# Performance work log

Measured on AMD Instinct MI355X. Metric: run time of the kernel, lower is better.

Reference implementation:

```python
import jax, jax.numpy as jnp
import numpy as np

ALPHA = 0.1


def path_layer(feats, paths, pw, fcW):
    # feats: (N, D); paths: (P, N, L); pw: (L, D); fcW: (D, D)
    gathered = feats[paths]                      # (P, N, L, D) gather
    r = jnp.einsum('pnld,ld->nd', gathered, pw) / paths.shape[0]
    return jax.nn.relu(r @ fcW)


def setup_inputs() -> dict:
    key = jax.random.key(0)
    ks = jax.random.split(key, 16)
    Nm, Nd, D = 8000, 6000, 128
    P, L1, L2, S = 8, 4, 6, 200000
    inp = {
        'paths_mm': jax.random.randint(ks[0], (P, Nm, L1), 0, Nm),
        'paths_dd': jax.random.randint(ks[1], (P, Nd, L1), 0, Nd),
        'paths_md': jax.random.randint(ks[2], (P, Nm + Nd, L2), 0, Nm + Nd),
        'miRNA': jax.random.normal(ks[3], (Nm, Nm), jnp.float32),
        'disease': jax.random.normal(ks[4], (Nd, Nd), jnp.float32),
        'samples': jax.random.randint(ks[5], (S, 2), 0, Nd),
        'Wm': jax.random.normal(ks[6], (Nm, D), jnp.float32) * 0.02,
        'Wd': jax.random.normal(ks[7], (Nd, D), jnp.float32) * 0.02,
        'pw1': jax.random.normal(ks[8], (2, L1, D), jnp.float32) * 0.5,
        'pw2': jax.random.normal(ks[9], (2, L2, D), jnp.float32) * 0.5,
        'fcW': jax.random.normal(ks[10], (2, D, D), jnp.float32) * 0.1,
        'mlpW0': jax.random.normal(ks[11], (4 * D, 256), jnp.float32) * 0.05,
        'mlpb0': jnp.zeros((256,), jnp.float32),
        'mlpW1': jax.random.normal(ks[12], (256, 64), jnp.float32) * 0.05,
        'mlpb1': jnp.zeros((64,), jnp.float32),
        'mlpW2': jax.random.normal(ks[13], (64, 1), jnp.float32) * 0.05,
        'mlpb2': jnp.zeros((1,), jnp.float32),
    }
    return inp


def reference(paths_mm, paths_dd, paths_md, miRNA, disease, samples,
              Wm, Wd, pw1, pw2, fcW, mlpW0, mlpb0, mlpW1, mlpb1, mlpW2, mlpb2):
    num_layers = fcW.shape[0]
    Nm = Wm.shape[0]

    init_m = miRNA @ Wm            # lin_m(miRNA): (Nm, D)
    init_d = disease @ Wd          # lin_d(disease): (Nd, D)

    feats_mm = init_m
    for l in range(num_layers):
        feats_mm = path_layer(feats_mm, paths_mm, pw1[l], fcW[l])
        feats_mm = ALPHA * init_m + (1.0 - ALPHA) * feats_mm

    feats_dd = init_d
    for l in range(num_layers):
        feats_dd = path_layer(feats_dd, paths_dd, pw1[l], fcW[l])
        feats_dd = ALPHA * init_d + (1.0 - ALPHA) * feats_dd

    init_md = jnp.concatenate([init_m, init_d], axis=0)   # (Nm+Nd, D)
    feats_md = init_md
    for l in range(num_layers):
        feats_md = path_layer(feats_md, paths_md, pw2[l], fcW[l])
        feats_md = ALPHA * init_md + (1.0 - ALPHA) * feats_md

    emb_mm = jnp.concatenate([feats_mm, feats_md[:Nm]], axis=1)   # (Nm, 2D)
    emb_dd = jnp.concatenate([feats_dd, feats_md[Nm:]], axis=1)   # (Nd, 2D)

    emb = jnp.concatenate([emb_mm[samples[:, 0]], emb_dd[samples[:, 1]]], axis=1)  # (S, 4D)

    h = jax.nn.relu if False else None  # torch mlp has no activations between linears
    x = emb @ mlpW0 + mlpb0
    x = x @ mlpW1 + mlpb1
    x = x @ mlpW2 + mlpb2
    return jax.nn.sigmoid(x)
```

## Files before the change

### kernel.cpp

```cpp
#include <hip/hip_runtime.h>
#include <hip/hip_bf16.h>
#include <cstdint>
#include <cstddef>

#define ALPHA_ 0.1f

static inline int cdiv(int a, int b) { return (a + b - 1) / b; }

typedef __attribute__((ext_vector_type(8))) short short8;
typedef __attribute__((ext_vector_type(4))) short short4v;
typedef __attribute__((ext_vector_type(4))) float float4v;

struct P8 { float* p[8]; };

__device__ __forceinline__ void gload_lds16(const void* g, void* l) {
  __builtin_amdgcn_global_load_lds((const __attribute__((address_space(1))) unsigned int*)g,
                                   (__attribute__((address_space(3))) unsigned int*)l,
                                   16, 0, 0);
}

__global__ __launch_bounds__(256) void make_wtT(const float* __restrict__ W,
                                                __hip_bfloat16* __restrict__ WtT,
                                                int K)
{
  __shared__ float tile[32][129];
  const int t  = threadIdx.x;
  const int s  = blockIdx.x;
  const int k0 = s * 32;
#pragma unroll
  for (int pass = 0; pass < 4; ++pass) {
    int idx = pass * 1024 + t * 4;
    int k = idx >> 7, c = idx & 127;
    float4v v;
    const float* src = W + (size_t)(k0 + k) * 128 + c;
    if (k0 + k < K) v = *(const float4v*)src;
    else            v = (float4v){0.f, 0.f, 0.f, 0.f};
    tile[k][c] = v.x; tile[k][c + 1] = v.y; tile[k][c + 2] = v.z; tile[k][c + 3] = v.w;
  }
  __syncthreads();
#pragma unroll
  for (int pass = 0; pass < 16; ++pass) {
    int idx = pass * 256 + t;
    int kg = idx >> 10, rem = idx & 1023;
    int c = rem >> 3, e = rem & 7;
    WtT[(size_t)s * 4096 + idx] = __float2bfloat16(tile[kg * 8 + e][c]);
  }
}

template<int KSPLIT>
__global__ __launch_bounds__(512) void init_mfma5(
    const float* __restrict__ Am, const __hip_bfloat16* __restrict__ Wtm, int Nm_, int nbm,
    const float* __restrict__ Ad, const __hip_bfloat16* __restrict__ Wtd, int Nd_, int Kpd,
    P8 parr)
{
  __shared__ __align__(16) __hip_bfloat16 lds_a[128 * 128];
  __shared__ __align__(16) __hip_bfloat16 lds_w[4 * 4096];

  const int t    = threadIdx.x;
  const int lane = t & 63;
  const int wv   = t >> 6;

  const int chunk = blockIdx.x % KSPLIT;
  int mb          = blockIdx.x / KSPLIT;

  const float* A; const __hip_bfloat16* Wt; int N, K, Kpad, rowoff, rb;
  if (mb < nbm) { A = Am; Wt = Wtm; N = Nm_; K = Nm_; Kpad = nbm * 128; rowoff = 0;   rb = mb; }
  else          { A = Ad; Wt = Wtd; N = Nd_; K = Nd_; Kpad = Kpd;       rowoff = Nm_; rb = mb - nbm; }

  float* Cp = parr.p[chunk];

  const int St = Kpad / 128;
  const int s0 = (int)(((long)St * chunk) / KSPLIT);
  const int s1 = (int)(((long)St * (chunk + 1)) / KSPLIT);

  const int row_g0 = rb * 128;

  const float* apass[8];
  int aw_byte[8];
#pragma unroll
  for (int p = 0; p < 8; ++p) {
    int f   = p * 512 + t;
    int row = f >> 5, kq = f & 31;
    int rg  = row_g0 + row; if (rg > N - 1) rg = N - 1;
    apass[p] = A + (size_t)rg * K + kq * 4;
    int c = kq >> 1, h = kq & 1;
    aw_byte[p] = row * 256 + ((c ^ (row & 15)) << 4) + h * 8;
  }

  const int rloc  = lane & 15;
  const int kg    = lane >> 4;
  const int row_l = wv * 16 + rloc;
  int a_rbyte[4];
#pragma unroll
  for (int sub = 0; sub < 4; ++sub) {
    int c = sub * 4 + kg;
    a_rbyte[sub] = row_l * 256 + ((c ^ (row_l & 15)) << 4);
  }
  int w_roff[8];
#pragma unroll
  for (int mt = 0; mt < 8; ++mt)
    w_roff[mt] = (mt * 16 + rloc) * 8;

  float4v acc[8];
#pragma unroll
  for (int mt = 0; mt < 8; ++mt) acc[mt] = (float4v){0.f, 0.f, 0.f, 0.f};

  const char* wt_bytes = (const char*)Wt;

  for (int s = s0; s < s1; ++s) {
#pragma unroll
    for (int i = 0; i < 4; ++i) {
      gload_lds16(wt_bytes + (size_t)(s * 4) * 8192 + (size_t)(i * 512 + wv * 64 + lane) * 16,
                  (char*)lds_w + (size_t)(i * 512 + wv * 64) * 16);
    }
    float4v av[8];
    const int kb = s * 128;
#pragma unroll
    for (int p = 0; p < 8; ++p) {
      const float* src = apass[p] + kb;
      ptrdiff_t rel = (src - A);
      av[p] = *(const float4v*)(A + ((rel > (ptrdiff_t)((size_t)(N) * K - 4)) ? ((size_t)N * K - 4) : rel));
    }
#pragma unroll
    for (int p = 0; p < 8; ++p) {
      union { short4v v; __hip_bfloat16 h[4]; } pk;
      pk.h[0] = __float2bfloat16(av[p].x); pk.h[1] = __float2bfloat16(av[p].y);
      pk.h[2] = __float2bfloat16(av[p].z); pk.h[3] = __float2bfloat16(av[p].w);
      *(short4v*)((char*)lds_a + aw_byte[p]) = pk.v;
    }
    __syncthreads();

#pragma unroll
    for (int sub = 0; sub < 4; ++sub) {
      short8 afrag = *(const short8*)((const char*)lds_a + a_rbyte[sub]);
      const __hip_bfloat16* lw = lds_w + sub * 4096 + kg * 1024;
#pragma unroll
      for (int mt = 0; mt < 8; ++mt) {
        short8 wfrag = *(const short8*)(lw + w_roff[mt]);
        acc[mt] = __builtin_amdgcn_mfma_f32_16x16x32_bf16(wfrag, afrag, acc[mt], 0, 0, 0);
      }
    }
    __syncthreads();
  }

  int row = row_g0 + row_l;
  if (row < N) {
    float* dst = Cp + (size_t)(rowoff + row) * 128 + kg * 4;
#pragma unroll
    for (int mt = 0; mt < 8; ++mt)
      *(float4v*)(dst + mt * 16) = acc[mt];
  }
}

template<int NP>
__global__ __launch_bounds__(256) void combineN(
    P8 parr, float4v* __restrict__ o_init, __hip_bfloat16* __restrict__ state,
    int n4, int NtD)
{
  int i = blockIdx.x * 256 + threadIdx.x;
  if (i >= n4) return;
  float4v s = ((const float4v*)parr.p[0])[i];
#pragma unroll
  for (int j = 1; j < NP; ++j) {
    float4v x = ((const float4v*)parr.p[j])[i];
    s.x += x.x; s.y += x.y; s.z += x.z; s.w += x.w;
  }
  o_init[i] = s;
  union { short4v v; __hip_bfloat16 h[4]; } b;
  b.h[0] = __float2bfloat16(s.x); b.h[1] = __float2bfloat16(s.y);
  b.h[2] = __float2bfloat16(s.z); b.h[3] = __float2bfloat16(s.w);
  *(short4v*)(state + (size_t)i * 4) = b.v;
  *(short4v*)(state + (size_t)NtD + (size_t)i * 4) = b.v;
}

template<int L, int PP>
__device__ __forceinline__ float gath(const __hip_bfloat16* __restrict__ sect,
                                      const int* __restrict__ paths,
                                      const float* __restrict__ pw, int n, int N, int d)
{
  float pwv[L];
#pragma unroll
  for (int l = 0; l < L; ++l) pwv[l] = pw[l * 128 + d];
  float acc = 0.f;
  const int* ip0 = paths + (size_t)n * L;
#pragma unroll
  for (int p = 0; p < PP; ++p) {
    const int* ip = ip0 + (size_t)p * N * L;
    int idx[L];
#pragma unroll
    for (int l = 0; l < L; ++l) idx[l] = ip[l];
#pragma unroll
    for (int l = 0; l < L; ++l)
      acc = fmaf(pwv[l], __bfloat162float(sect[(size_t)idx[l] * 128 + d]), acc);
  }
  return acc;
}

template<int LMM, int LMD, int PP>
__global__ __launch_bounds__(256) void layer_fused(
    const __hip_bfloat16* __restrict__ stateIn,
    const int* __restrict__ paths_mm, const int* __restrict__ paths_dd, const int* __restrict__ paths_md,
    const float* __restrict__ pw1l, const float* __restrict__ pw2l,
    const float* __restrict__ fcWl, const float* __restrict__ initb,
    __hip_bfloat16* __restrict__ stateOut,
    int Nm, int Nd, int nbm, int nbd)
{
  __shared__ float r_lds[16][128];
  const int t  = threadIdx.x;
  const int Nt = Nm + Nd;
  int b = blockIdx.x;

  const __hip_bfloat16* sect; const int* paths; const float* pw;
  int N, rowbase, nb; bool md;
  if (b < nbm)            { sect = stateIn;                     paths = paths_mm; pw = pw1l; N = Nm; rowbase = 0;  nb = b;             md = false; }
  else if (b < nbm + nbd) { sect = stateIn + (size_t)Nm * 128;  paths = paths_dd; pw = pw1l; N = Nd; rowbase = Nm; nb = b - nbm;       md = false; }
  else                    { sect = stateIn + (size_t)Nt * 128;  paths = paths_md; pw = pw2l; N = Nt; rowbase = Nt; nb = b - nbm - nbd; md = true;  }

  const int d   = t & 127;
  const int sub = t >> 7;
  const int n0  = nb * 16;

#pragma unroll
  for (int i = 0; i < 8; ++i) {
    int slot = sub + 2 * i;
    int n = n0 + slot;
    int ng = (n < N) ? n : (N - 1);
    float acc = md ? gath<LMD, PP>(sect, paths, pw, ng, N, d)
                   : gath<LMM, PP>(sect, paths, pw, ng, N, d);
    r_lds[slot][d] = acc * (1.0f / (float)PP);
  }
  __syncthreads();

  const int col = d;
  const int rh  = sub;
  float acc2[8];
#pragma unroll
  for (int j = 0; j < 8; ++j) acc2[j] = 0.f;
#pragma unroll 4
  for (int k = 0; k < 128; k += 8) {
    float w[8];
#pragma unroll
    for (int kk = 0; kk < 8; ++kk) w[kk] = fcWl[(size_t)(k + kk) * 128 + col];
#pragma unroll
    for (int j = 0; j < 8; ++j) {
      const float* rp = &r_lds[rh * 8 + j][k];
#pragma unroll
      for (int kk = 0; kk < 8; ++kk) acc2[j] = fmaf(rp[kk], w[kk], acc2[j]);
    }
  }
#pragma unroll
  for (int j = 0; j < 8; ++j) {
    int n = n0 + rh * 8 + j;
    if (n < N) {
      int rr = rowbase + n;
      int rbase = (rr < Nt) ? rr : rr - Nt;
      float v = ALPHA_ * initb[(size_t)rbase * 128 + col] + (1.f - ALPHA_) * fmaxf(acc2[j], 0.f);
      stateOut[(size_t)rr * 128 + col] = __float2bfloat16(v);
    }
  }
}

__global__ __launch_bounds__(256) void gather_einsum_rt(
    const __hip_bfloat16* __restrict__ feats, const int* __restrict__ paths,
    const float* __restrict__ pw, float* __restrict__ r, int N, int P, int L)
{
  const int d = threadIdx.x & 127;
  const int n = blockIdx.x * 2 + (threadIdx.x >> 7);
  if (n >= N) return;
  float acc = 0.f;
  for (int p = 0; p < P; ++p) {
    const int* ip = paths + ((size_t)p * N + n) * L;
    for (int l = 0; l < L; ++l)
      acc = fmaf(pw[l * 128 + d], __bfloat162float(feats[(size_t)ip[l] * 128 + d]), acc);
  }
  r[(size_t)n * 128 + d] = acc * (1.0f / (float)P);
}

template<int TR>
__global__ __launch_bounds__(256) void fc_all(
    const float* __restrict__ Rm, const float* __restrict__ W,
    const float* __restrict__ initb, __hip_bfloat16* __restrict__ state, int Ntot, int Nt)
{
  const int col = threadIdx.x & 127;
  const int rh  = __builtin_amdgcn_readfirstlane((int)(threadIdx.x >> 7));
  const int row0 = blockIdx.x * (2 * TR) + rh * TR;
  const float* arow[TR];
#pragma unroll
  for (int r = 0; r < TR; ++r) {
    int rr = row0 + r; if (rr > Ntot - 1) rr = Ntot - 1;
    arow[r] = Rm + (size_t)rr * 128;
  }
  float acc[TR];
#pragma unroll
  for (int r = 0; r < TR; ++r) acc[r] = 0.f;
#pragma unroll 4
  for (int k = 0; k < 128; k += 8) {
    float w[8];
#pragma unroll
    for (int kk = 0; kk < 8; ++kk) w[kk] = W[(size_t)(k + kk) * 128 + col];
#pragma unroll
    for (int r = 0; r < TR; ++r) {
      const float* ap = arow[r] + k;
#pragma unroll
      for (int kk = 0; kk < 8; ++kk) acc[r] = fmaf(ap[kk], w[kk], acc[r]);
    }
  }
#pragma unroll
  for (int r = 0; r < TR; ++r) {
    int rr = row0 + r;
    if (rr < Ntot) {
      int rbase = (rr < Nt) ? rr : rr - Nt;
      float v = ALPHA_ * initb[(size_t)rbase * 128 + col] + (1.f - ALPHA_) * fmaxf(acc[r], 0.f);
      state[(size_t)rr * 128 + col] = __float2bfloat16(v);
    }
  }
}

__global__ void collapse1(const float* __restrict__ W0, const float* __restrict__ b0,
                          const float* __restrict__ W1, const float* __restrict__ b1,
                          float* __restrict__ w01, float* __restrict__ b01,
                          int E, int K0, int H1)
{
  int row = blockIdx.x; int c = threadIdx.x;
  if (c >= H1) return;
  const float* src; float base;
  if (row < E) { src = W0 + (size_t)row * K0; base = 0.f; }
  else         { src = b0; base = b1[c]; }
  float a0 = 0.f, a1 = 0.f, a2 = 0.f, a3 = 0.f;
#pragma unroll 4
  for (int k = 0; k < K0; k += 4) {
    a0 = fmaf(src[k + 0], W1[(size_t)(k + 0) * H1 + c], a0);
    a1 = fmaf(src[k + 1], W1[(size_t)(k + 1) * H1 + c], a1);
    a2 = fmaf(src[k + 2], W1[(size_t)(k + 2) * H1 + c], a2);
    a3 = fmaf(src[k + 3], W1[(size_t)(k + 3) * H1 + c], a3);
  }
  float acc = base + ((a0 + a1) + (a2 + a3));
  if (row < E) w01[(size_t)row * H1 + c] = acc; else b01[c] = acc;
}

__global__ void collapse2(const float* __restrict__ w01, const float* __restrict__ b01,
                          const float* __restrict__ W2, const float* __restrict__ b2,
                          float* __restrict__ w512, float* __restrict__ csc,
                          int E, int H1)
{
  int i = blockIdx.x * blockDim.x + threadIdx.x;
  if (i < E) {
    float a0 = 0.f, a1 = 0.f, a2 = 0.f, a3 = 0.f;
    for (int j = 0; j < H1; j += 4) {
      a0 = fmaf(w01[(size_t)i * H1 + j + 0], W2[j + 0], a0);
      a1 = fmaf(w01[(size_t)i * H1 + j + 1], W2[j + 1], a1);
      a2 = fmaf(w01[(size_t)i * H1 + j + 2], W2[j + 2], a2);
      a3 = fmaf(w01[(size_t)i * H1 + j + 3], W2[j + 3], a3);
    }
    w512[i] = (a0 + a1) + (a2 + a3);
  } else if (i == E) {
    float a = b2[0];
    for (int j = 0; j < H1; ++j) a = fmaf(b01[j], W2[j], a);
    csc[0] = a;
  }
}

__global__ __launch_bounds__(256) void node_partial(
    const __hip_bfloat16* __restrict__ Fmm, const __hip_bfloat16* __restrict__ Fdd,
    const __hip_bfloat16* __restrict__ Fmd,
    const float* __restrict__ w512, float* __restrict__ uv, int Nm, int Nt)
{
  int gid = blockIdx.x * blockDim.x + threadIdx.x;
  int wid = gid >> 6;
  int lane = threadIdx.x & 63;
  if (wid >= Nt) return;
  bool isM = wid < Nm;
  const __hip_bfloat16* X = isM ? (Fmm + (size_t)wid * 128) : (Fdd + (size_t)(wid - Nm) * 128);
  const __hip_bfloat16* Y = Fmd + (size_t)wid * 128;
  const float* w1 = w512 + (isM ? 0 : 256);
  const float* w2 = w1 + 128;
  float s = __bfloat162float(X[lane]) * w1[lane];
  s = fmaf(__bfloat162float(X[lane + 64]), w1[lane + 64], s);
  s = fmaf(__bfloat162float(Y[lane]), w2[lane], s);
  s = fmaf(__bfloat162float(Y[lane + 64]), w2[lane + 64], s);
#pragma unroll
  for (int off = 32; off > 0; off >>= 1) s += __shfl_down(s, off);
  if (lane == 0) uv[wid] = s;
}

__global__ __launch_bounds__(256) void score_kernel(
    const int* __restrict__ samples, const float* __restrict__ u, const float* __restrict__ v,
    const float* __restrict__ csc, float* __restrict__ out, int S)
{
  int s = blockIdx.x * blockDim.x + threadIdx.x;
  if (s >= S) return;
  const int2 ij = ((const int2*)samples)[s];
  float x = u[ij.x] + v[ij.y] + csc[0];
  out[s] = 1.0f / (1.0f + expf(-x));
}

extern "C" void kernel_launch(void* const* d_in, const int* in_sizes, int n_in,
                              void* d_out, int out_size, void* d_ws, size_t ws_size,
                              hipStream_t stream)
{
  const int*   paths_mm = (const int*)d_in[0];
  const int*   paths_dd = (const int*)d_in[1];
  const int*   paths_md = (const int*)d_in[2];
  const float* miRNA    = (const float*)d_in[3];
  const float* disease  = (const float*)d_in[4];
  const int*   samples  = (const int*)d_in[5];
  const float* Wm  = (const float*)d_in[6];
  const float* Wd  = (const float*)d_in[7];
  const float* pw1 = (const float*)d_in[8];
  const float* pw2 = (const float*)d_in[9];
  const float* fcW = (const float*)d_in[10];
  const float* W0  = (const float*)d_in[11];
  const float* b0  = (const float*)d_in[12];
  const float* W1  = (const float*)d_in[13];
  const float* b1  = (const float*)d_in[14];
  const float* W2  = (const float*)d_in[15];
  const float* b2  = (const float*)d_in[16];

  const int D  = 128;
  const int Nm = in_sizes[6] / D;
  const int Nd = in_sizes[7] / D;
  const int Nt = Nm + Nd;
  const int S  = in_sizes[5] / 2;
  const int layers = in_sizes[10] / (D * D);
  const int L1 = in_sizes[8] / (layers * D);
  const int L2 = in_sizes[9] / (layers * D);
  const int P  = in_sizes[0] / (Nm * L1);
  const int E  = 4 * D;
  const int K0 = in_sizes[12];
  const int H1 = in_sizes[14];
  const int Kpm = cdiv(Nm, 128) * 128;
  const int Kpd = cdiv(Nd, 128) * 128;
  const size_t NtD = (size_t)Nt * D;

  float* out = (float*)d_out;
  float* ws  = (float*)d_ws;
  size_t off = 0;
  float* init   = ws + off; off += NtD;
  __hip_bfloat16* stateA = (__hip_bfloat16*)(ws + off); off += NtD;
  __hip_bfloat16* stateB = (__hip_bfloat16*)(ws + off); off += NtD;
  float* w01    = ws + off; off += (size_t)E * H1;
  float* b01    = ws + off; off += H1;
  float* w512   = ws + off; off += E;
  float* csc    = ws + off; off += 1;
  float* uv     = ws + off; off += Nt;
  __hip_bfloat16* WtTm = (__hip_bfloat16*)(ws + off); off += (size_t)D * Kpm / 2;
  __hip_bfloat16* WtTd = (__hip_bfloat16*)(ws + off); off += (size_t)D * Kpd / 2;
  float* pextra = ws + off;
  const bool big_ws = (off + 3 * NtD) * 4 <= ws_size;
  (void)n_in; (void)out_size;

  make_wtT<<<Kpm / 32, 256, 0, stream>>>(Wm, WtTm, Nm);
  make_wtT<<<Kpd / 32, 256, 0, stream>>>(Wd, WtTd, Nd);

  collapse1<<<E + 1, 64, 0, stream>>>(W0, b0, W1, b1, w01, b01, E, K0, H1);
  collapse2<<<cdiv(E + 1, 256), 256, 0, stream>>>(w01, b01, W2, b2, w512, csc, E, H1);

  {
    int nbm = Kpm / 128, nbd = cdiv(Nd, 128);
    int n4 = (int)(NtD / 4);
    P8 parr;
    parr.p[0] = init;
    parr.p[1] = (float*)stateB;
    if (big_ws) {
      parr.p[2] = pextra;
      parr.p[3] = pextra + NtD;
      parr.p[4] = pextra + 2 * NtD;
      init_mfma5<5><<<(nbm + nbd) * 5, 512, 0, stream>>>(
          miRNA, WtTm, Nm, nbm, disease, WtTd, Nd, Kpd, parr);
      combineN<5><<<cdiv(n4, 256), 256, 0, stream>>>(parr, (float4v*)init, stateA, n4, (int)NtD);
    } else {
      parr.p[2] = pextra;
      init_mfma5<3><<<(nbm + nbd) * 3, 512, 0, stream>>>(
          miRNA, WtTm, Nm, nbm, disease, WtTd, Nd, Kpd, parr);
      combineN<3><<<cdiv(n4, 256), 256, 0, stream>>>(parr, (float4v*)init, stateA, n4, (int)NtD);
    }
  }

  const bool fuse_ok = (L1 == 4 && L2 == 6 && P == 8 &&
                        Nm % 16 == 0 && Nd % 16 == 0 && Nt % 16 == 0);
  __hip_bfloat16* cur = stateA;
  __hip_bfloat16* nxt = stateB;
  for (int l = 0; l < layers; ++l) {
    const float* pw1l = pw1 + (size_t)l * L1 * D;
    const float* pw2l = pw2 + (size_t)l * L2 * D;
    const float* fcWl = fcW + (size_t)l * D * D;
    if (fuse_ok) {
      int nbm16 = Nm / 16, nbd16 = Nd / 16, nbt16 = Nt / 16;
      layer_fused<4, 6, 8><<<nbm16 + nbd16 + nbt16, 256, 0, stream>>>(
          cur, paths_mm, paths_dd, paths_md, pw1l, pw2l, fcWl, init, nxt,
          Nm, Nd, nbm16, nbd16);
    } else {
      float* bufR = pextra;
      gather_einsum_rt<<<cdiv(Nm, 2), 256, 0, stream>>>(cur, paths_mm, pw1l, bufR, Nm, P, L1);
      gather_einsum_rt<<<cdiv(Nd, 2), 256, 0, stream>>>(cur + (size_t)Nm * D, paths_dd, pw1l,
                                                        bufR + (size_t)Nm * D, Nd, P, L1);
      gather_einsum_rt<<<cdiv(Nt, 2), 256, 0, stream>>>(cur + NtD, paths_md, pw2l,
                                                        bufR + NtD, Nt, P, L2);
      fc_all<8><<<cdiv(2 * Nt, 16), 256, 0, stream>>>(
          bufR, fcWl, init, nxt, 2 * Nt, Nt);
    }
    __hip_bfloat16* tmp = cur; cur = nxt; nxt = tmp;
  }

  node_partial<<<cdiv(Nt * 64, 256), 256, 0, stream>>>(
      cur, cur + (size_t)Nm * D, cur + NtD, w512, uv, Nm, Nt);
  score_kernel<<<cdiv(S, 256), 256, 0, stream>>>(samples, uv, uv + Nm, csc, out, S);
}
```

Measured before the change: 278.3 us.

## Retile init GEMM to 256-row blocks with 64-wide K steps and deeper split-K

```diff
diff --git a/kernel.cpp b/kernel.cpp
--- a/kernel.cpp
+++ b/kernel.cpp
@@ -11,7 +11,7 @@
 typedef __attribute__((ext_vector_type(4))) short short4v;
 typedef __attribute__((ext_vector_type(4))) float float4v;
 
-struct P8 { float* p[8]; };
+struct P12 { float* p[12]; };
 
 __device__ __forceinline__ void gload_lds16(const void* g, void* l) {
   __builtin_amdgcn_global_load_lds((const __attribute__((address_space(1))) unsigned int*)g,
@@ -48,13 +48,13 @@
 }
 
 template<int KSPLIT>
-__global__ __launch_bounds__(512) void init_mfma5(
-    const float* __restrict__ Am, const __hip_bfloat16* __restrict__ Wtm, int Nm_, int nbm,
+__global__ __launch_bounds__(512, 4) void init_mfma6(
+    const float* __restrict__ Am, const __hip_bfloat16* __restrict__ Wtm, int Nm_, int nbm, int Kpm,
     const float* __restrict__ Ad, const __hip_bfloat16* __restrict__ Wtd, int Nd_, int Kpd,
-    P8 parr)
-{
-  __shared__ __align__(16) __hip_bfloat16 lds_a[128 * 128];
-  __shared__ __align__(16) __hip_bfloat16 lds_w[4 * 4096];
+    P12 parr)
+{
+  __shared__ __align__(16) __hip_bfloat16 lds_a[256 * 64];
+  __shared__ __align__(16) __hip_bfloat16 lds_w[2 * 4096];
 
   const int t    = threadIdx.x;
   const int lane = t & 63;
@@ -64,62 +64,66 @@
   int mb          = blockIdx.x / KSPLIT;
 
   const float* A; const __hip_bfloat16* Wt; int N, K, Kpad, rowoff, rb;
-  if (mb < nbm) { A = Am; Wt = Wtm; N = Nm_; K = Nm_; Kpad = nbm * 128; rowoff = 0;   rb = mb; }
-  else          { A = Ad; Wt = Wtd; N = Nd_; K = Nd_; Kpad = Kpd;       rowoff = Nm_; rb = mb - nbm; }
+  if (mb < nbm) { A = Am; Wt = Wtm; N = Nm_; K = Nm_; Kpad = Kpm; rowoff = 0;   rb = mb; }
+  else          { A = Ad; Wt = Wtd; N = Nd_; K = Nd_; Kpad = Kpd; rowoff = Nm_; rb = mb - nbm; }
 
   float* Cp = parr.p[chunk];
 
-  const int St = Kpad / 128;
+  const int St = Kpad / 64;
   const int s0 = (int)(((long)St * chunk) / KSPLIT);
   const int s1 = (int)(((long)St * (chunk + 1)) / KSPLIT);
 
-  const int row_g0 = rb * 128;
+  const int row_g0 = rb * 256;
 
   const float* apass[8];
   int aw_byte[8];
 #pragma unroll
   for (int p = 0; p < 8; ++p) {
     int f   = p * 512 + t;
-    int row = f >> 5, kq = f & 31;
+    int row = f >> 4, kq = f & 15;
     int rg  = row_g0 + row; if (rg > N - 1) rg = N - 1;
     apass[p] = A + (size_t)rg * K + kq * 4;
     int c = kq >> 1, h = kq & 1;
-    aw_byte[p] = row * 256 + ((c ^ (row & 15)) << 4) + h * 8;
-  }
-
-  const int rloc  = lane & 15;
-  const int kg    = lane >> 4;
-  const int row_l = wv * 16 + rloc;
-  int a_rbyte[4];
-#pragma unroll
-  for (int sub = 0; sub < 4; ++sub) {
-    int c = sub * 4 + kg;
-    a_rbyte[sub] = row_l * 256 + ((c ^ (row_l & 15)) << 4);
+    aw_byte[p] = row * 128 + ((c ^ (row & 7)) << 4) + h * 8;
+  }
+
+  const int rloc = lane & 15;
+  const int kg   = lane >> 4;
+  int a_rbyte[2][2];
+#pragma unroll
+  for (int g = 0; g < 2; ++g) {
+    int row_l = wv * 32 + g * 16 + rloc;
+#pragma unroll
+    for (int sub = 0; sub < 2; ++sub) {
+      int c = sub * 4 + kg;
+      a_rbyte[g][sub] = row_l * 128 + ((c ^ (row_l & 7)) << 4);
+    }
   }
   int w_roff[8];
 #pragma unroll
   for (int mt = 0; mt < 8; ++mt)
     w_roff[mt] = (mt * 16 + rloc) * 8;
 
-  float4v acc[8];
-#pragma unroll
-  for (int mt = 0; mt < 8; ++mt) acc[mt] = (float4v){0.f, 0.f, 0.f, 0.f};
+  float4v accA[8], accB[8];
+#pragma unroll
+  for (int mt = 0; mt < 8; ++mt) { accA[mt] = (float4v){0,0,0,0}; accB[mt] = (float4v){0,0,0,0}; }
 
   const char* wt_bytes = (const char*)Wt;
+  const size_t amax = (size_t)N * K - 4;
 
   for (int s = s0; s < s1; ++s) {
 #pragma unroll
-    for (int i = 0; i < 4; ++i) {
-      gload_lds16(wt_bytes + (size_t)(s * 4) * 8192 + (size_t)(i * 512 + wv * 64 + lane) * 16,
-                  (char*)lds_w + (size_t)(i * 512 + wv * 64) * 16);
+    for (int i = 0; i < 2; ++i) {
+      gload_lds16(wt_bytes + (size_t)(s * 2 + i) * 8192 + (size_t)t * 16,
+                  (char*)lds_w + (size_t)i * 8192 + (size_t)(wv * 64) * 16);
     }
     float4v av[8];
-    const int kb = s * 128;
+    const int kb = s * 64;
 #pragma unroll
     for (int p = 0; p < 8; ++p) {
       const float* src = apass[p] + kb;
-      ptrdiff_t rel = (src - A);
-      av[p] = *(const float4v*)(A + ((rel > (ptrdiff_t)((size_t)(N) * K - 4)) ? ((size_t)N * K - 4) : rel));
+      ptrdiff_t rel = src - A;
+      av[p] = *(const float4v*)(A + (((size_t)rel > amax) ? amax : (size_t)rel));
     }
 #pragma unroll
     for (int p = 0; p < 8; ++p) {
@@ -131,30 +135,35 @@
     __syncthreads();
 
 #pragma unroll
-    for (int sub = 0; sub < 4; ++sub) {
-      short8 afrag = *(const short8*)((const char*)lds_a + a_rbyte[sub]);
+    for (int sub = 0; sub < 2; ++sub) {
+      short8 afA = *(const short8*)((const char*)lds_a + a_rbyte[0][sub]);
+      short8 afB = *(const short8*)((const char*)lds_a + a_rbyte[1][sub]);
       const __hip_bfloat16* lw = lds_w + sub * 4096 + kg * 1024;
 #pragma unroll
       for (int mt = 0; mt < 8; ++mt) {
         short8 wfrag = *(const short8*)(lw + w_roff[mt]);
-        acc[mt] = __builtin_amdgcn_mfma_f32_16x16x32_bf16(wfrag, afrag, acc[mt], 0, 0, 0);
+        accA[mt] = __builtin_amdgcn_mfma_f32_16x16x32_bf16(wfrag, afA, accA[mt], 0, 0, 0);
+        accB[mt] = __builtin_amdgcn_mfma_f32_16x16x32_bf16(wfrag, afB, accB[mt], 0, 0, 0);
       }
     }
     __syncthreads();
   }
 
-  int row = row_g0 + row_l;
-  if (row < N) {
-    float* dst = Cp + (size_t)(rowoff + row) * 128 + kg * 4;
-#pragma unroll
-    for (int mt = 0; mt < 8; ++mt)
-      *(float4v*)(dst + mt * 16) = acc[mt];
+#pragma unroll
+  for (int g = 0; g < 2; ++g) {
+    int row = row_g0 + wv * 32 + g * 16 + rloc;
+    if (row < N) {
+      float* dst = Cp + (size_t)(rowoff + row) * 128 + kg * 4;
+#pragma unroll
+      for (int mt = 0; mt < 8; ++mt)
+        *(float4v*)(dst + mt * 16) = (g == 0) ? accA[mt] : accB[mt];
+    }
   }
 }
 
 template<int NP>
 __global__ __launch_bounds__(256) void combineN(
-    P8 parr, float4v* __restrict__ o_init, __hip_bfloat16* __restrict__ state,
+    P12 parr, float4v* __restrict__ o_init, __hip_bfloat16* __restrict__ state,
     int n4, int NtD)
 {
   int i = blockIdx.x * 256 + threadIdx.x;
@@ -428,8 +437,8 @@
   const int E  = 4 * D;
   const int K0 = in_sizes[12];
   const int H1 = in_sizes[14];
-  const int Kpm = cdiv(Nm, 128) * 128;
-  const int Kpd = cdiv(Nd, 128) * 128;
+  const int Kpm = cdiv(Nm, 64) * 64;
+  const int Kpd = cdiv(Nd, 64) * 64;
   const size_t NtD = (size_t)Nt * D;
 
   float* out = (float*)d_out;
@@ -446,7 +455,6 @@
   __hip_bfloat16* WtTm = (__hip_bfloat16*)(ws + off); off += (size_t)D * Kpm / 2;
   __hip_bfloat16* WtTd = (__hip_bfloat16*)(ws + off); off += (size_t)D * Kpd / 2;
   float* pextra = ws + off;
-  const bool big_ws = (off + 3 * NtD) * 4 <= ws_size;
   (void)n_in; (void)out_size;
 
   make_wtT<<<Kpm / 32, 256, 0, stream>>>(Wm, WtTm, Nm);
@@ -456,22 +464,23 @@
   collapse2<<<cdiv(E + 1, 256), 256, 0, stream>>>(w01, b01, W2, b2, w512, csc, E, H1);
 
   {
-    int nbm = Kpm / 128, nbd = cdiv(Nd, 128);
+    int nbm = cdiv(Nm, 256), nbd = cdiv(Nd, 256);
     int n4 = (int)(NtD / 4);
-    P8 parr;
+    P12 parr;
     parr.p[0] = init;
     parr.p[1] = (float*)stateB;
-    if (big_ws) {
-      parr.p[2] = pextra;
-      parr.p[3] = pextra + NtD;
-      parr.p[4] = pextra + 2 * NtD;
-      init_mfma5<5><<<(nbm + nbd) * 5, 512, 0, stream>>>(
-          miRNA, WtTm, Nm, nbm, disease, WtTd, Nd, Kpd, parr);
-      combineN<5><<<cdiv(n4, 256), 256, 0, stream>>>(parr, (float4v*)init, stateA, n4, (int)NtD);
+    for (int j = 0; j < 10; ++j) parr.p[2 + j] = pextra + (size_t)j * NtD;
+    if ((off + 7 * NtD) * 4 <= ws_size) {
+      init_mfma6<9><<<(nbm + nbd) * 9, 512, 0, stream>>>(
+          miRNA, WtTm, Nm, nbm, Kpm, disease, WtTd, Nd, Kpd, parr);
+      combineN<9><<<cdiv(n4, 256), 256, 0, stream>>>(parr, (float4v*)init, stateA, n4, (int)NtD);
+    } else if ((off + 4 * NtD) * 4 <= ws_size) {
+      init_mfma6<6><<<(nbm + nbd) * 6, 512, 0, stream>>>(
+          miRNA, WtTm, Nm, nbm, Kpm, disease, WtTd, Nd, Kpd, parr);
+      combineN<6><<<cdiv(n4, 256), 256, 0, stream>>>(parr, (float4v*)init, stateA, n4, (int)NtD);
     } else {
-      parr.p[2] = pextra;
-      init_mfma5<3><<<(nbm + nbd) * 3, 512, 0, stream>>>(
-          miRNA, WtTm, Nm, nbm, disease, WtTd, Nd, Kpd, parr);
+      init_mfma6<3><<<(nbm + nbd) * 3, 512, 0, stream>>>(
+          miRNA, WtTm, Nm, nbm, Kpm, disease, WtTd, Nd, Kpd, parr);
       combineN<3><<<cdiv(n4, 256), 256, 0, stream>>>(parr, (float4v*)init, stateA, n4, (int)NtD);
     }
   }
```

After: 270.2 us, median of 2. 1.03x faster.
